# Performance work log

Hardware: AMD Instinct MI355X
Metric: run time of the kernel (lower is better)

The kernel has to match this reference:

```python
import jax, jax.numpy as jnp
import numpy as np

N_QUBITS = 10
N_LAYERS = 3
OUT_MIN, OUT_MAX = -0.1, 0.1


def _apply_1q(state, U, wire):
    # state: (B, 2**n) complex64; U: (2,2) complex64 gate on `wire` (wire 0 = MSB, PennyLane order)
    B = state.shape[0]
    s = state.reshape(B, 2 ** wire, 2, -1)
    s = jnp.einsum('ij,bljr->blir', U, s)
    return s.reshape(B, -1)


def _apply_ry_batched(state, theta, wire):
    # per-sample RY(theta) on `wire`; theta: (B,)
    B = state.shape[0]
    s = state.reshape(B, 2 ** wire, 2, -1)
    c = jnp.cos(0.5 * theta)[:, None, None]
    si = jnp.sin(0.5 * theta)[:, None, None]
    a0, a1 = s[:, :, 0, :], s[:, :, 1, :]
    s = jnp.stack([c * a0 - si * a1, si * a0 + c * a1], axis=2)
    return s.reshape(B, -1)


def _apply_cnot(state, ctrl):
    # CNOT with control=ctrl, target=ctrl+1 (adjacent wires)
    B = state.shape[0]
    s = state.reshape(B, 2 ** ctrl, 2, 2, -1)
    s = jnp.stack([s[:, :, 0], s[:, :, 1, ::-1]], axis=2)
    return s.reshape(B, -1)


def _circuit(z, weights):
    # Faithful statevector simulation of the PennyLane qnode, batched over samples.
    B = z.shape[0]
    n = N_QUBITS
    state = jnp.zeros((B, 2 ** n), jnp.complex64).at[:, 0].set(1.0)
    zc = jnp.clip(z, -1.0, 1.0)
    for i in range(n):
        state = _apply_ry_batched(state, zc[:, i % zc.shape[1]], i)
    # Fuse RZ(a)->RY(b)->RZ(c) per (layer, qubit) into one 2x2 unitary: U = Rz(c) @ Ry(b) @ Rz(a)
    a, b, c = weights[..., 0], weights[..., 1], weights[..., 2]
    ea, eap = jnp.exp(-0.5j * a), jnp.exp(0.5j * a)
    ec, ecp = jnp.exp(-0.5j * c), jnp.exp(0.5j * c)
    cb, sb = jnp.cos(0.5 * b), jnp.sin(0.5 * b)
    U = jnp.stack([jnp.stack([ec * cb * ea, -ec * sb * eap], -1),
                   jnp.stack([ecp * sb * ea, ecp * cb * eap], -1)], -2)  # (L, Q, 2, 2)
    U = U.astype(jnp.complex64)
    for l in range(N_LAYERS):
        for i in range(n):
            state = _apply_1q(state, U[l, i], i)
        for i in range(n - 1):
            state = _apply_cnot(state, i)
    probs = jnp.abs(state) ** 2  # (B, 2**n) float32
    feats = []
    for i in range(n):
        p = probs.reshape(B, 2 ** i, 2, -1)
        feats.append(p[:, :, 0].sum((1, 2)) - p[:, :, 1].sum((1, 2)))  # <Z_i>
    return jnp.stack(feats, -1)  # (B, n_qubits)


def setup_inputs() -> dict:
    key = jax.random.key(0)
    ks = jax.random.split(key, 8)
    B = 4096
    return {
        'z': jax.random.normal(ks[0], (B, N_QUBITS), jnp.float32),
        'weights': jax.random.normal(ks[1], (N_LAYERS, N_QUBITS, 3), jnp.float32) * 0.01,
        'W1': jax.random.normal(ks[2], (N_QUBITS, 32), jnp.float32) * 0.3,
        'b1': jax.random.normal(ks[3], (32,), jnp.float32) * 0.05,
        'W2': jax.random.normal(ks[4], (32, 16), jnp.float32) * 0.2,
        'b2': jax.random.normal(ks[5], (16,), jnp.float32) * 0.05,
        'W3': jax.random.normal(ks[6], (16, 1), jnp.float32) * 0.2,
        'b3': jax.random.normal(ks[7], (1,), jnp.float32) * 0.05,
    }


def reference(z, weights, W1, b1, W2, b2, W3, b3):
    feats = _circuit(z, weights)                  # (B, n_qubits)
    h = jnp.tanh(feats @ W1 + b1)
    h = jnp.tanh(h @ W2 + b2)
    raw = h @ W3 + b3                             # (B, 1)
    return jax.nn.sigmoid(raw) * (OUT_MAX - OUT_MIN) + OUT_MIN
```

## Files before the change

### kernel.cpp

```cpp
#include <hip/hip_runtime.h>

namespace {

constexpr int NQ = 10;

struct cplx { float re, im; };

__device__ __forceinline__ cplx cmul(cplx a, cplx b) {
  cplx r;
  r.re = fmaf(a.re, b.re, -a.im * b.im);
  r.im = fmaf(a.re, b.im,  a.im * b.re);
  return r;
}

__device__ __forceinline__ cplx cmadd2(cplx u, cplx a, cplx v, cplx b) {
  cplx r;
  r.re = fmaf(u.re, a.re, fmaf(-u.im, a.im, fmaf(v.re, b.re, -v.im * b.im)));
  r.im = fmaf(u.re, a.im, fmaf( u.im, a.re, fmaf(v.re, b.im,  v.im * b.re)));
  return r;
}

__device__ __forceinline__ cplx csel(bool c, cplx x, cplx y) {
  cplx r; r.re = c ? x.re : y.re; r.im = c ? x.im : y.im; return r;
}

__device__ __forceinline__ float fast_tanh(float x) {
  float xc = fminf(fmaxf(x, -10.f), 10.f);
  float e = __expf(2.f * xc);
  return __fdividef(e - 1.f, e + 1.f);
}

template<int CTRL>
__device__ __forceinline__ float dppf(float v) {
  return __int_as_float(__builtin_amdgcn_update_dpp(0, __float_as_int(v), CTRL, 0xF, 0xF, true));
}
template<int CTRL>
__device__ __forceinline__ cplx dppc(cplx v) { return { dppf<CTRL>(v.re), dppf<CTRL>(v.im) }; }

__device__ __forceinline__ cplx shflxc(cplx v, int m) {
  cplx r; r.re = __shfl_xor(v.re, m); r.im = __shfl_xor(v.im, m); return r;
}

__device__ __forceinline__ float rdlane(float v, int l) {
  return __int_as_float(__builtin_amdgcn_readlane(__float_as_int(v), l));
}

__device__ __forceinline__ float wave_sum(float v) {
  v += dppf<0xB1>(v);
  v += dppf<0x4E>(v);
  v += __shfl_xor(v, 4);
  v += dppf<0x128>(v);
  v += __shfl_xor(v, 16);
  return rdlane(v, 0) + rdlane(v, 32);
}

__device__ __forceinline__ void loadU(const float* __restrict__ Ut, int g,
                                      cplx& u00, cplx& u01, cplx& u10, cplx& u11) {
  const float* p = Ut + g * 8;
  u00 = {p[0], p[1]}; u01 = {p[2], p[3]};
  u10 = {p[4], p[5]}; u11 = {p[6], p[7]};
}

template<int LX, int HIL>
__device__ __forceinline__ void laneGateDS(cplx (&amp)[16], int lane,
    cplx u00, cplx u01, cplx u10, cplx u11) {
  bool hi = (__popc(lane & HIL) & 1) != 0;
  cplx cA = csel(hi, u11, u00), cB = csel(hi, u10, u01);
  #pragma unroll
  for (int t = 0; t < 16; ++t) {
    cplx o = shflxc(amp[t], LX);
    amp[t] = cmadd2(cA, amp[t], cB, o);
  }
}

template<int CTRL, int HIL>
__device__ __forceinline__ void laneGateDPP(cplx (&amp)[16], int lane,
    cplx u00, cplx u01, cplx u10, cplx u11) {
  bool hi = (__popc(lane & HIL) & 1) != 0;
  cplx cA = csel(hi, u11, u00), cB = csel(hi, u10, u01);
  #pragma unroll
  for (int t = 0; t < 16; ++t) {
    cplx o = dppc<CTRL>(amp[t]);
    amp[t] = cmadd2(cA, amp[t], cB, o);
  }
}

template<int CTRL, int LOCX, int HIL>
__device__ __forceinline__ void mixedGate(cplx (&amp)[16], int lane,
    cplx u00, cplx u01, cplx u10, cplx u11) {
  bool hi = (__popc(lane & HIL) & 1) != 0;
  cplx cA = csel(hi, u11, u00), cB = csel(hi, u10, u01);
  #pragma unroll
  for (int t0 = 0; t0 < 16; ++t0) {
    if (t0 & LOCX) continue;
    const int t1 = t0 | LOCX;
    cplx o0 = dppc<CTRL>(amp[t1]);
    cplx o1 = dppc<CTRL>(amp[t0]);
    amp[t0] = cmadd2(cA, amp[t0], cB, o0);
    amp[t1] = cmadd2(cA, amp[t1], cB, o1);
  }
}

constexpr int hbit(int m) { return m >= 8 ? 8 : (m >= 4 ? 4 : (m >= 2 ? 2 : 1)); }

template<int PLOC, int HIL, int HILOC>
__device__ __forceinline__ void localGate(cplx (&amp)[16], int lane,
    cplx u00, cplx u01, cplx u10, cplx u11) {
  bool h0 = (__popc(lane & HIL) & 1) != 0;
  cplx cA0 = csel(h0, u11, u00), cB0 = csel(h0, u10, u01);
  cplx cA1 = csel(h0, u00, u11), cB1 = csel(h0, u01, u10);
  #pragma unroll
  for (int ta = 0; ta < 16; ++ta) {
    if (ta & hbit(PLOC)) continue;
    const int tb = ta ^ PLOC;
    const bool pa = (__popc(ta & HILOC) & 1) != 0;
    cplx aA = amp[ta], aB = amp[tb];
    if (!pa) {
      amp[ta] = cmadd2(cA0, aA, cB0, aB);
      amp[tb] = cmadd2(cA1, aB, cB1, aA);
    } else {
      amp[ta] = cmadd2(cA1, aA, cB1, aB);
      amp[tb] = cmadd2(cA0, aB, cB0, aA);
    }
  }
}

__global__ void qgan_prep(const float* __restrict__ wts, float* __restrict__ U) {
  int g = threadIdx.x;
  if (g >= 30) return;
  float a = wts[g * 3 + 0], b = wts[g * 3 + 1], c = wts[g * 3 + 2];
  float al = 0.5f * (a + c), be = 0.5f * (a - c), hb = 0.5f * b;
  float ca = cosf(al), sa = sinf(al);
  float cbe = cosf(be), sbe = sinf(be);
  float cb = cosf(hb), sb = sinf(hb);
  float* p = U + g * 8;
  p[0] =  cb * ca;  p[1] = -cb * sa;
  p[2] = -sb * cbe; p[3] = -sb * sbe;
  p[4] =  sb * cbe; p[5] = -sb * sbe;
  p[6] =  cb * ca;  p[7] =  cb * sa;
}

__global__ __launch_bounds__(256, 4)
void qgan_kernel(const float* __restrict__ z, const float* __restrict__ Ut,
                 const float* __restrict__ W1, const float* __restrict__ b1,
                 const float* __restrict__ W2, const float* __restrict__ b2,
                 const float* __restrict__ W3, const float* __restrict__ b3,
                 float* __restrict__ out, int B)
{
  const int tid  = blockIdx.x * 256 + threadIdx.x;
  const int lane = threadIdx.x & 63;
  const int wv   = __builtin_amdgcn_readfirstlane(tid >> 6);
  if (wv >= B) return;

  cplx u00, u01, u10, u11;

  cplx laneF = {1.f, 0.f};
  #pragma unroll
  for (int q = 0; q < 6; ++q) {
    float zz = z[wv * NQ + q];
    zz = fminf(fmaxf(zz, -1.f), 1.f);
    float c0 = __cosf(0.5f * zz), s0 = __sinf(0.5f * zz);
    loadU(Ut, q, u00, u01, u10, u11);
    cplx va = { fmaf(u00.re, c0, u01.re * s0), fmaf(u00.im, c0, u01.im * s0) };
    cplx vb = { fmaf(u10.re, c0, u11.re * s0), fmaf(u10.im, c0, u11.im * s0) };
    cplx f = ((lane >> (5 - q)) & 1) ? vb : va;
    laneF = (q == 0) ? f : cmul(laneF, f);
  }
  cplx va_[4], vb_[4];
  #pragma unroll
  for (int q = 6; q < 10; ++q) {
    float zz = z[wv * NQ + q];
    zz = fminf(fmaxf(zz, -1.f), 1.f);
    float c0 = __cosf(0.5f * zz), s0 = __sinf(0.5f * zz);
    loadU(Ut, q, u00, u01, u10, u11);
    va_[q - 6] = { fmaf(u00.re, c0, u01.re * s0), fmaf(u00.im, c0, u01.im * s0) };
    vb_[q - 6] = { fmaf(u10.re, c0, u11.re * s0), fmaf(u10.im, c0, u11.im * s0) };
  }

  cplx amp[16];
  {
    cplx P2[4];
    P2[0] = cmul(va_[2], va_[3]);
    P2[1] = cmul(va_[2], vb_[3]);
    P2[2] = cmul(vb_[2], va_[3]);
    P2[3] = cmul(vb_[2], vb_[3]);
    cplx g0 = cmul(laneF, va_[0]);
    cplx g1 = cmul(laneF, vb_[0]);
    #pragma unroll
    for (int t = 0; t < 16; ++t) {
      cplx t7 = ((t >> 2) & 1) ? vb_[1] : va_[1];
      cplx tt = cmul(t7, P2[t & 3]);
      amp[t] = cmul(((t >> 3) & 1) ? g1 : g0, tt);
    }
  }

  loadU(Ut, 10, u00,u01,u10,u11); laneGateDS <0x30, 0x20>(amp, lane, u00,u01,u10,u11);
  loadU(Ut, 11, u00,u01,u10,u11); laneGateDS <0x18, 0x30>(amp, lane, u00,u01,u10,u11);
  loadU(Ut, 12, u00,u01,u10,u11); laneGateDS <0x0C, 0x38>(amp, lane, u00,u01,u10,u11);
  loadU(Ut, 13, u00,u01,u10,u11); laneGateDS <0x06, 0x3C>(amp, lane, u00,u01,u10,u11);
  loadU(Ut, 14, u00,u01,u10,u11); laneGateDPP<0x1B, 0x3E>(amp, lane, u00,u01,u10,u11);
  loadU(Ut, 15, u00,u01,u10,u11); mixedGate  <0xB1, 8, 0x3F>(amp, lane, u00,u01,u10,u11);
  loadU(Ut, 16, u00,u01,u10,u11); localGate  <0xC, 0x3F, 0x8>(amp, lane, u00,u01,u10,u11);
  loadU(Ut, 17, u00,u01,u10,u11); localGate  <0x6, 0x3F, 0xC>(amp, lane, u00,u01,u10,u11);
  loadU(Ut, 18, u00,u01,u10,u11); localGate  <0x3, 0x3F, 0xE>(amp, lane, u00,u01,u10,u11);
  loadU(Ut, 19, u00,u01,u10,u11); localGate  <0x1, 0x3F, 0xF>(amp, lane, u00,u01,u10,u11);

  loadU(Ut, 20, u00,u01,u10,u11); laneGateDS <0x28, 0x20>(amp, lane, u00,u01,u10,u11);
  loadU(Ut, 21, u00,u01,u10,u11); laneGateDS <0x14, 0x10>(amp, lane, u00,u01,u10,u11);
  loadU(Ut, 22, u00,u01,u10,u11); laneGateDS <0x0A, 0x28>(amp, lane, u00,u01,u10,u11);
  loadU(Ut, 23, u00,u01,u10,u11); laneGateDS <0x05, 0x14>(amp, lane, u00,u01,u10,u11);
  loadU(Ut, 24, u00,u01,u10,u11); mixedGate  <0x4E, 8, 0x2A>(amp, lane, u00,u01,u10,u11);
  loadU(Ut, 25, u00,u01,u10,u11); mixedGate  <0xB1, 4, 0x15>(amp, lane, u00,u01,u10,u11);
  loadU(Ut, 26, u00,u01,u10,u11); localGate  <0xA, 0x2A, 0x8>(amp, lane, u00,u01,u10,u11);
  loadU(Ut, 27, u00,u01,u10,u11); localGate  <0x5, 0x15, 0x4>(amp, lane, u00,u01,u10,u11);
  loadU(Ut, 28, u00,u01,u10,u11); localGate  <0x2, 0x2A, 0xA>(amp, lane, u00,u01,u10,u11);
  loadU(Ut, 29, u00,u01,u10,u11); localGate  <0x1, 0x15, 0x5>(amp, lane, u00,u01,u10,u11);

  float p[16];
  #pragma unroll
  for (int t = 0; t < 16; ++t)
    p[t] = fmaf(amp[t].re, amp[t].re, amp[t].im * amp[t].im);

  float s0 = 0.f, s8 = 0.f, sC = 0.f, s6 = 0.f, s3 = 0.f;
  #pragma unroll
  for (int t = 0; t < 16; ++t) {
    s0 += p[t];
    s8 += (__popc(t & 0x8) & 1) ? -p[t] : p[t];
    sC += (__popc(t & 0xC) & 1) ? -p[t] : p[t];
    s6 += (__popc(t & 0x6) & 1) ? -p[t] : p[t];
    s3 += (__popc(t & 0x3) & 1) ? -p[t] : p[t];
  }

  const int   lmask[10] = {0x20,0x30,0x18,0x0C,0x26,0x33,0x19,0x0C,0x26,0x33};
  const float lsrc[10]  = {s0,  s0,  s0,  s0,  s0,  s0,  s8,  sC,  s6,  s3 };
  float feats[10];
  #pragma unroll
  for (int w = 0; w < 10; ++w) {
    int par = __popc(lane & lmask[w]) & 1;
    float v = __int_as_float(__float_as_int(lsrc[w]) ^ (par << 31));
    feats[w] = wave_sum(v);
  }

  const int j = lane & 31;
  float acc = b1[j];
  #pragma unroll
  for (int i = 0; i < NQ; ++i) acc = fmaf(feats[i], W1[i * 32 + j], acc);
  float h1 = fast_tanh(acc);

  const int k = lane & 15;
  float acc2 = b2[k];
  #pragma unroll
  for (int jj = 0; jj < 32; ++jj)
    acc2 = fmaf(rdlane(h1, jj), W2[jj * 16 + k], acc2);
  float h2 = fast_tanh(acc2);

  float vv = h2 * W3[k];
  vv += dppf<0xB1>(vv);
  vv += dppf<0x4E>(vv);
  vv += __shfl_xor(vv, 4);
  vv += dppf<0x128>(vv);

  if (lane == 0) out[wv] = 0.1f * fast_tanh(0.5f * (vv + b3[0]));
}

}

extern "C" void kernel_launch(void* const* d_in, const int* in_sizes, int n_in,
                              void* d_out, int out_size, void* d_ws, size_t ws_size,
                              hipStream_t stream) {
  const float* z   = (const float*)d_in[0];
  const float* wts = (const float*)d_in[1];
  const float* W1  = (const float*)d_in[2];
  const float* b1  = (const float*)d_in[3];
  const float* W2  = (const float*)d_in[4];
  const float* b2  = (const float*)d_in[5];
  const float* W3  = (const float*)d_in[6];
  const float* b3  = (const float*)d_in[7];
  float* out = (float*)d_out;
  float* U   = (float*)d_ws;

  int B = in_sizes[0] / NQ;
  hipLaunchKernelGGL(qgan_prep, dim3(1), dim3(32), 0, stream, wts, U);
  int blocks = (B + 3) / 4;
  hipLaunchKernelGGL(qgan_kernel, dim3(blocks), dim3(256), 0, stream,
                     z, U, W1, b1, W2, b2, W3, b3, out, B);
}
```

Before: 93.29 us.

## Use packed float2 math, DPP/swizzle lane exchanges, and fold gate prep into kernel

Complex arithmetic is rewritten on two-wide float vectors so the compiler can emit packed FMA instructions. Several cross-lane shuffles (ds_bpermute-based) are replaced with ds_swizzle or chained DPP moves. The separate prep kernel that built the gate unitaries is removed: each wave computes them per lane and broadcasts them with readlane, which saves a launch and the global loads at the cost of redundant trig per wave. The reductions also swap one shuffle for DPP.

```diff
diff --git a/kernel.cpp b/kernel.cpp
--- a/kernel.cpp
+++ b/kernel.cpp
@@ -4,24 +4,125 @@
 
 constexpr int NQ = 10;
 
-struct cplx { float re, im; };
-
-__device__ __forceinline__ cplx cmul(cplx a, cplx b) {
-  cplx r;
-  r.re = fmaf(a.re, b.re, -a.im * b.im);
-  r.im = fmaf(a.re, b.im,  a.im * b.re);
+typedef float v2f __attribute__((ext_vector_type(2)));
+
+__device__ __forceinline__ float rdlane(float v, int l) {
+  return __int_as_float(__builtin_amdgcn_readlane(__float_as_int(v), l));
+}
+template<int CTRL>
+__device__ __forceinline__ float dppf(float v) {
+  return __int_as_float(__builtin_amdgcn_update_dpp(0, __float_as_int(v), CTRL, 0xF, 0xF, true));
+}
+template<int CTRL>
+__device__ __forceinline__ v2f dppv(v2f v) { return v2f{dppf<CTRL>(v.x), dppf<CTRL>(v.y)}; }
+template<int C1, int C2>
+__device__ __forceinline__ v2f dppv2(v2f v) { return dppv<C2>(dppv<C1>(v)); }
+
+template<int PAT>
+__device__ __forceinline__ v2f swzv(v2f v) {
+  return v2f{ __int_as_float(__builtin_amdgcn_ds_swizzle(__float_as_int(v.x), PAT)),
+              __int_as_float(__builtin_amdgcn_ds_swizzle(__float_as_int(v.y), PAT)) };
+}
+__device__ __forceinline__ v2f shflx(v2f v, int m) {
+  return v2f{ __shfl_xor(v.x, m), __shfl_xor(v.y, m) };
+}
+
+__device__ __forceinline__ v2f pfma(v2f a, v2f b, v2f c) { return __builtin_elementwise_fma(a, b, c); }
+__device__ __forceinline__ v2f swp(v2f a) { return v2f{a.y, a.x}; }
+__device__ __forceinline__ v2f cmulv(v2f a, v2f b) {
+  return pfma(swp(b), v2f{-a.y, a.y}, b * v2f{a.x, a.x});
+}
+__device__ __forceinline__ v2f vsel(bool c, v2f a, v2f b) {
+  return v2f{ c ? a.x : b.x, c ? a.y : b.y };
+}
+struct pkco { v2f rA, iA, rB, iB; };
+__device__ __forceinline__ pkco mkco(v2f cA, v2f cB) {
+  return pkco{ v2f{cA.x, cA.x}, v2f{-cA.y, cA.y}, v2f{cB.x, cB.x}, v2f{-cB.y, cB.y} };
+}
+__device__ __forceinline__ v2f capply(const pkco& c, v2f a, v2f o) {
+  v2f r = a * c.rA;
+  r = pfma(swp(a), c.iA, r);
+  r = pfma(o, c.rB, r);
+  r = pfma(swp(o), c.iB, r);
   return r;
 }
 
-__device__ __forceinline__ cplx cmadd2(cplx u, cplx a, cplx v, cplx b) {
-  cplx r;
-  r.re = fmaf(u.re, a.re, fmaf(-u.im, a.im, fmaf(v.re, b.re, -v.im * b.im)));
-  r.im = fmaf(u.re, a.im, fmaf( u.im, a.re, fmaf(v.re, b.im,  v.im * b.re)));
-  return r;
-}
-
-__device__ __forceinline__ cplx csel(bool c, cplx x, cplx y) {
-  cplx r; r.re = c ? x.re : y.re; r.im = c ? x.im : y.im; return r;
+__device__ __forceinline__ float wave_sum(float v) {
+  v += dppf<0xB1>(v);
+  v += dppf<0x4E>(v);
+  v += dppf<0x1B>(dppf<0x141>(v));
+  v += dppf<0x128>(v);
+  v += __shfl_xor(v, 16);
+  return rdlane(v, 0) + rdlane(v, 32);
+}
+
+struct Umat { float r00,i00,r01,i01,r10,i10,r11,i11; };
+__device__ __forceinline__ void getU(const Umat& m, int g,
+                                     v2f& u00, v2f& u01, v2f& u10, v2f& u11) {
+  u00 = v2f{rdlane(m.r00, g), rdlane(m.i00, g)};
+  u01 = v2f{rdlane(m.r01, g), rdlane(m.i01, g)};
+  u10 = v2f{rdlane(m.r10, g), rdlane(m.i10, g)};
+  u11 = v2f{rdlane(m.r11, g), rdlane(m.i11, g)};
+}
+
+template<int HIL>
+__device__ __forceinline__ pkco gateco(int lane, v2f u00, v2f u01, v2f u10, v2f u11) {
+  bool hi = (__popc(lane & HIL) & 1) != 0;
+  return mkco(vsel(hi, u11, u00), vsel(hi, u10, u01));
+}
+
+template<int LX, int HIL>
+__device__ __forceinline__ void gate_shfl(v2f (&amp)[16], int lane, v2f u00,v2f u01,v2f u10,v2f u11) {
+  pkco c = gateco<HIL>(lane, u00,u01,u10,u11);
+  #pragma unroll
+  for (int t = 0; t < 16; ++t) amp[t] = capply(c, amp[t], shflx(amp[t], LX));
+}
+template<int PAT, int HIL>
+__device__ __forceinline__ void gate_swz(v2f (&amp)[16], int lane, v2f u00,v2f u01,v2f u10,v2f u11) {
+  pkco c = gateco<HIL>(lane, u00,u01,u10,u11);
+  #pragma unroll
+  for (int t = 0; t < 16; ++t) amp[t] = capply(c, amp[t], swzv<PAT>(amp[t]));
+}
+template<int C1, int HIL>
+__device__ __forceinline__ void gate_dpp1(v2f (&amp)[16], int lane, v2f u00,v2f u01,v2f u10,v2f u11) {
+  pkco c = gateco<HIL>(lane, u00,u01,u10,u11);
+  #pragma unroll
+  for (int t = 0; t < 16; ++t) amp[t] = capply(c, amp[t], dppv<C1>(amp[t]));
+}
+template<int C1, int C2, int HIL>
+__device__ __forceinline__ void gate_dpp2(v2f (&amp)[16], int lane, v2f u00,v2f u01,v2f u10,v2f u11) {
+  pkco c = gateco<HIL>(lane, u00,u01,u10,u11);
+  #pragma unroll
+  for (int t = 0; t < 16; ++t) amp[t] = capply(c, amp[t], dppv2<C1,C2>(amp[t]));
+}
+template<int CTRL, int LOCX, int HIL>
+__device__ __forceinline__ void gate_mixed(v2f (&amp)[16], int lane, v2f u00,v2f u01,v2f u10,v2f u11) {
+  pkco c = gateco<HIL>(lane, u00,u01,u10,u11);
+  #pragma unroll
+  for (int t0 = 0; t0 < 16; ++t0) {
+    if (t0 & LOCX) continue;
+    const int t1 = t0 | LOCX;
+    v2f o0 = dppv<CTRL>(amp[t1]);
+    v2f o1 = dppv<CTRL>(amp[t0]);
+    amp[t0] = capply(c, amp[t0], o0);
+    amp[t1] = capply(c, amp[t1], o1);
+  }
+}
+constexpr int hbit(int m) { return m >= 8 ? 8 : (m >= 4 ? 4 : (m >= 2 ? 2 : 1)); }
+template<int PLOC, int HIL, int HILOC>
+__device__ __forceinline__ void gate_local(v2f (&amp)[16], int lane, v2f u00,v2f u01,v2f u10,v2f u11) {
+  bool h0 = (__popc(lane & HIL) & 1) != 0;
+  pkco c0 = mkco(vsel(h0, u11, u00), vsel(h0, u10, u01));
+  pkco c1 = mkco(vsel(h0, u00, u11), vsel(h0, u01, u10));
+  #pragma unroll
+  for (int ta = 0; ta < 16; ++ta) {
+    if (ta & hbit(PLOC)) continue;
+    const int tb = ta ^ PLOC;
+    const bool pa = (__popc(ta & HILOC) & 1) != 0;
+    v2f aA = amp[ta], aB = amp[tb];
+    if (!pa) { amp[ta] = capply(c0, aA, aB); amp[tb] = capply(c1, aB, aA); }
+    else     { amp[ta] = capply(c1, aA, aB); amp[tb] = capply(c0, aB, aA); }
+  }
 }
 
 __device__ __forceinline__ float fast_tanh(float x) {
@@ -30,118 +131,8 @@
   return __fdividef(e - 1.f, e + 1.f);
 }
 
-template<int CTRL>
-__device__ __forceinline__ float dppf(float v) {
-  return __int_as_float(__builtin_amdgcn_update_dpp(0, __float_as_int(v), CTRL, 0xF, 0xF, true));
-}
-template<int CTRL>
-__device__ __forceinline__ cplx dppc(cplx v) { return { dppf<CTRL>(v.re), dppf<CTRL>(v.im) }; }
-
-__device__ __forceinline__ cplx shflxc(cplx v, int m) {
-  cplx r; r.re = __shfl_xor(v.re, m); r.im = __shfl_xor(v.im, m); return r;
-}
-
-__device__ __forceinline__ float rdlane(float v, int l) {
-  return __int_as_float(__builtin_amdgcn_readlane(__float_as_int(v), l));
-}
-
-__device__ __forceinline__ float wave_sum(float v) {
-  v += dppf<0xB1>(v);
-  v += dppf<0x4E>(v);
-  v += __shfl_xor(v, 4);
-  v += dppf<0x128>(v);
-  v += __shfl_xor(v, 16);
-  return rdlane(v, 0) + rdlane(v, 32);
-}
-
-__device__ __forceinline__ void loadU(const float* __restrict__ Ut, int g,
-                                      cplx& u00, cplx& u01, cplx& u10, cplx& u11) {
-  const float* p = Ut + g * 8;
-  u00 = {p[0], p[1]}; u01 = {p[2], p[3]};
-  u10 = {p[4], p[5]}; u11 = {p[6], p[7]};
-}
-
-template<int LX, int HIL>
-__device__ __forceinline__ void laneGateDS(cplx (&amp)[16], int lane,
-    cplx u00, cplx u01, cplx u10, cplx u11) {
-  bool hi = (__popc(lane & HIL) & 1) != 0;
-  cplx cA = csel(hi, u11, u00), cB = csel(hi, u10, u01);
-  #pragma unroll
-  for (int t = 0; t < 16; ++t) {
-    cplx o = shflxc(amp[t], LX);
-    amp[t] = cmadd2(cA, amp[t], cB, o);
-  }
-}
-
-template<int CTRL, int HIL>
-__device__ __forceinline__ void laneGateDPP(cplx (&amp)[16], int lane,
-    cplx u00, cplx u01, cplx u10, cplx u11) {
-  bool hi = (__popc(lane & HIL) & 1) != 0;
-  cplx cA = csel(hi, u11, u00), cB = csel(hi, u10, u01);
-  #pragma unroll
-  for (int t = 0; t < 16; ++t) {
-    cplx o = dppc<CTRL>(amp[t]);
-    amp[t] = cmadd2(cA, amp[t], cB, o);
-  }
-}
-
-template<int CTRL, int LOCX, int HIL>
-__device__ __forceinline__ void mixedGate(cplx (&amp)[16], int lane,
-    cplx u00, cplx u01, cplx u10, cplx u11) {
-  bool hi = (__popc(lane & HIL) & 1) != 0;
-  cplx cA = csel(hi, u11, u00), cB = csel(hi, u10, u01);
-  #pragma unroll
-  for (int t0 = 0; t0 < 16; ++t0) {
-    if (t0 & LOCX) continue;
-    const int t1 = t0 | LOCX;
-    cplx o0 = dppc<CTRL>(amp[t1]);
-    cplx o1 = dppc<CTRL>(amp[t0]);
-    amp[t0] = cmadd2(cA, amp[t0], cB, o0);
-    amp[t1] = cmadd2(cA, amp[t1], cB, o1);
-  }
-}
-
-constexpr int hbit(int m) { return m >= 8 ? 8 : (m >= 4 ? 4 : (m >= 2 ? 2 : 1)); }
-
-template<int PLOC, int HIL, int HILOC>
-__device__ __forceinline__ void localGate(cplx (&amp)[16], int lane,
-    cplx u00, cplx u01, cplx u10, cplx u11) {
-  bool h0 = (__popc(lane & HIL) & 1) != 0;
-  cplx cA0 = csel(h0, u11, u00), cB0 = csel(h0, u10, u01);
-  cplx cA1 = csel(h0, u00, u11), cB1 = csel(h0, u01, u10);
-  #pragma unroll
-  for (int ta = 0; ta < 16; ++ta) {
-    if (ta & hbit(PLOC)) continue;
-    const int tb = ta ^ PLOC;
-    const bool pa = (__popc(ta & HILOC) & 1) != 0;
-    cplx aA = amp[ta], aB = amp[tb];
-    if (!pa) {
-      amp[ta] = cmadd2(cA0, aA, cB0, aB);
-      amp[tb] = cmadd2(cA1, aB, cB1, aA);
-    } else {
-      amp[ta] = cmadd2(cA1, aA, cB1, aB);
-      amp[tb] = cmadd2(cA0, aB, cB0, aA);
-    }
-  }
-}
-
-__global__ void qgan_prep(const float* __restrict__ wts, float* __restrict__ U) {
-  int g = threadIdx.x;
-  if (g >= 30) return;
-  float a = wts[g * 3 + 0], b = wts[g * 3 + 1], c = wts[g * 3 + 2];
-  float al = 0.5f * (a + c), be = 0.5f * (a - c), hb = 0.5f * b;
-  float ca = cosf(al), sa = sinf(al);
-  float cbe = cosf(be), sbe = sinf(be);
-  float cb = cosf(hb), sb = sinf(hb);
-  float* p = U + g * 8;
-  p[0] =  cb * ca;  p[1] = -cb * sa;
-  p[2] = -sb * cbe; p[3] = -sb * sbe;
-  p[4] =  sb * cbe; p[5] = -sb * sbe;
-  p[6] =  cb * ca;  p[7] =  cb * sa;
-}
-
 __global__ __launch_bounds__(256, 4)
-void qgan_kernel(const float* __restrict__ z, const float* __restrict__ Ut,
+void qgan_kernel(const float* __restrict__ z, const float* __restrict__ wts,
                  const float* __restrict__ W1, const float* __restrict__ b1,
                  const float* __restrict__ W2, const float* __restrict__ b2,
                  const float* __restrict__ W3, const float* __restrict__ b3,
@@ -152,75 +143,89 @@
   const int wv   = __builtin_amdgcn_readfirstlane(tid >> 6);
   if (wv >= B) return;
 
-  cplx u00, u01, u10, u11;
-
-  cplx laneF = {1.f, 0.f};
+  Umat m;
+  {
+    int g = (lane < 30) ? lane : 0;
+    float wa = wts[g * 3 + 0], wb = wts[g * 3 + 1], wc = wts[g * 3 + 2];
+    float al = 0.5f * (wa + wc), be = 0.5f * (wa - wc), hb = 0.5f * wb;
+    float ca = __cosf(al),  sa = __sinf(al);
+    float cbe = __cosf(be), sbe = __sinf(be);
+    float cb = __cosf(hb),  sb = __sinf(hb);
+    m.r00 =  cb * ca;  m.i00 = -cb * sa;
+    m.r01 = -sb * cbe; m.i01 = -sb * sbe;
+    m.r10 =  sb * cbe; m.i10 = -sb * sbe;
+    m.r11 =  cb * ca;  m.i11 =  cb * sa;
+  }
+
+  v2f u00, u01, u10, u11;
+  const float* zp = z + wv * NQ;
+
+  v2f laneF = {1.f, 0.f};
   #pragma unroll
   for (int q = 0; q < 6; ++q) {
-    float zz = z[wv * NQ + q];
-    zz = fminf(fmaxf(zz, -1.f), 1.f);
+    float zz = fminf(fmaxf(zp[q], -1.f), 1.f);
     float c0 = __cosf(0.5f * zz), s0 = __sinf(0.5f * zz);
-    loadU(Ut, q, u00, u01, u10, u11);
-    cplx va = { fmaf(u00.re, c0, u01.re * s0), fmaf(u00.im, c0, u01.im * s0) };
-    cplx vb = { fmaf(u10.re, c0, u11.re * s0), fmaf(u10.im, c0, u11.im * s0) };
-    cplx f = ((lane >> (5 - q)) & 1) ? vb : va;
-    laneF = (q == 0) ? f : cmul(laneF, f);
-  }
-  cplx va_[4], vb_[4];
+    getU(m, q, u00, u01, u10, u11);
+    v2f va = pfma(u01, v2f{s0, s0}, u00 * v2f{c0, c0});
+    v2f vb = pfma(u11, v2f{s0, s0}, u10 * v2f{c0, c0});
+    v2f f = vsel((lane >> (5 - q)) & 1, vb, va);
+    laneF = (q == 0) ? f : cmulv(laneF, f);
+  }
+  v2f va_[4], vb_[4];
   #pragma unroll
   for (int q = 6; q < 10; ++q) {
-    float zz = z[wv * NQ + q];
-    zz = fminf(fmaxf(zz, -1.f), 1.f);
+    float zz = fminf(fmaxf(zp[q], -1.f), 1.f);
     float c0 = __cosf(0.5f * zz), s0 = __sinf(0.5f * zz);
-    loadU(Ut, q, u00, u01, u10, u11);
-    va_[q - 6] = { fmaf(u00.re, c0, u01.re * s0), fmaf(u00.im, c0, u01.im * s0) };
-    vb_[q - 6] = { fmaf(u10.re, c0, u11.re * s0), fmaf(u10.im, c0, u11.im * s0) };
-  }
-
-  cplx amp[16];
+    getU(m, q, u00, u01, u10, u11);
+    va_[q - 6] = pfma(u01, v2f{s0, s0}, u00 * v2f{c0, c0});
+    vb_[q - 6] = pfma(u11, v2f{s0, s0}, u10 * v2f{c0, c0});
+  }
+
+  v2f amp[16];
   {
-    cplx P2[4];
-    P2[0] = cmul(va_[2], va_[3]);
-    P2[1] = cmul(va_[2], vb_[3]);
-    P2[2] = cmul(vb_[2], va_[3]);
-    P2[3] = cmul(vb_[2], vb_[3]);
-    cplx g0 = cmul(laneF, va_[0]);
-    cplx g1 = cmul(laneF, vb_[0]);
+    v2f P2[4];
+    P2[0] = cmulv(va_[2], va_[3]);
+    P2[1] = cmulv(va_[2], vb_[3]);
+    P2[2] = cmulv(vb_[2], va_[3]);
+    P2[3] = cmulv(vb_[2], vb_[3]);
+    v2f g0 = cmulv(laneF, va_[0]);
+    v2f g1 = cmulv(laneF, vb_[0]);
     #pragma unroll
     for (int t = 0; t < 16; ++t) {
-      cplx t7 = ((t >> 2) & 1) ? vb_[1] : va_[1];
-      cplx tt = cmul(t7, P2[t & 3]);
-      amp[t] = cmul(((t >> 3) & 1) ? g1 : g0, tt);
+      v2f t7 = ((t >> 2) & 1) ? vb_[1] : va_[1];
+      v2f tt = cmulv(t7, P2[t & 3]);
+      amp[t] = cmulv(((t >> 3) & 1) ? g1 : g0, tt);
     }
   }
 
-  loadU(Ut, 10, u00,u01,u10,u11); laneGateDS <0x30, 0x20>(amp, lane, u00,u01,u10,u11);
-  loadU(Ut, 11, u00,u01,u10,u11); laneGateDS <0x18, 0x30>(amp, lane, u00,u01,u10,u11);
-  loadU(Ut, 12, u00,u01,u10,u11); laneGateDS <0x0C, 0x38>(amp, lane, u00,u01,u10,u11);
-  loadU(Ut, 13, u00,u01,u10,u11); laneGateDS <0x06, 0x3C>(amp, lane, u00,u01,u10,u11);
-  loadU(Ut, 14, u00,u01,u10,u11); laneGateDPP<0x1B, 0x3E>(amp, lane, u00,u01,u10,u11);
-  loadU(Ut, 15, u00,u01,u10,u11); mixedGate  <0xB1, 8, 0x3F>(amp, lane, u00,u01,u10,u11);
-  loadU(Ut, 16, u00,u01,u10,u11); localGate  <0xC, 0x3F, 0x8>(amp, lane, u00,u01,u10,u11);
-  loadU(Ut, 17, u00,u01,u10,u11); localGate  <0x6, 0x3F, 0xC>(amp, lane, u00,u01,u10,u11);
-  loadU(Ut, 18, u00,u01,u10,u11); localGate  <0x3, 0x3F, 0xE>(amp, lane, u00,u01,u10,u11);
-  loadU(Ut, 19, u00,u01,u10,u11); localGate  <0x1, 0x3F, 0xF>(amp, lane, u00,u01,u10,u11);
-
-  loadU(Ut, 20, u00,u01,u10,u11); laneGateDS <0x28, 0x20>(amp, lane, u00,u01,u10,u11);
-  loadU(Ut, 21, u00,u01,u10,u11); laneGateDS <0x14, 0x10>(amp, lane, u00,u01,u10,u11);
-  loadU(Ut, 22, u00,u01,u10,u11); laneGateDS <0x0A, 0x28>(amp, lane, u00,u01,u10,u11);
-  loadU(Ut, 23, u00,u01,u10,u11); laneGateDS <0x05, 0x14>(amp, lane, u00,u01,u10,u11);
-  loadU(Ut, 24, u00,u01,u10,u11); mixedGate  <0x4E, 8, 0x2A>(amp, lane, u00,u01,u10,u11);
-  loadU(Ut, 25, u00,u01,u10,u11); mixedGate  <0xB1, 4, 0x15>(amp, lane, u00,u01,u10,u11);
-  loadU(Ut, 26, u00,u01,u10,u11); localGate  <0xA, 0x2A, 0x8>(amp, lane, u00,u01,u10,u11);
-  loadU(Ut, 27, u00,u01,u10,u11); localGate  <0x5, 0x15, 0x4>(amp, lane, u00,u01,u10,u11);
-  loadU(Ut, 28, u00,u01,u10,u11); localGate  <0x2, 0x2A, 0xA>(amp, lane, u00,u01,u10,u11);
-  loadU(Ut, 29, u00,u01,u10,u11); localGate  <0x1, 0x15, 0x5>(amp, lane, u00,u01,u10,u11);
+  getU(m, 10, u00,u01,u10,u11); gate_shfl <0x30, 0x20>(amp, lane, u00,u01,u10,u11);
+  getU(m, 11, u00,u01,u10,u11); gate_swz  <0x601F, 0x30>(amp, lane, u00,u01,u10,u11);
+  getU(m, 12, u00,u01,u10,u11); gate_dpp2 <0x140, 0x1B, 0x38>(amp, lane, u00,u01,u10,u11);
+  getU(m, 13, u00,u01,u10,u11); gate_dpp2 <0x141, 0xB1, 0x3C>(amp, lane, u00,u01,u10,u11);
+  getU(m, 14, u00,u01,u10,u11); gate_dpp1 <0x1B, 0x3E>(amp, lane, u00,u01,u10,u11);
+  getU(m, 15, u00,u01,u10,u11); gate_mixed<0xB1, 8, 0x3F>(amp, lane, u00,u01,u10,u11);
+  getU(m, 16, u00,u01,u10,u11); gate_local<0xC, 0x3F, 0x8>(amp, lane, u00,u01,u10,u11);
+  getU(m, 17, u00,u01,u10,u11); gate_local<0x6, 0x3F, 0xC>(amp, lane, u00,u01,u10,u11);
+  getU(m, 18, u00,u01,u10,u11); gate_local<0x3, 0x3F, 0xE>(amp, lane, u00,u01,u10,u11);
+  getU(m, 19, u00,u01,u10,u11); gate_local<0x1, 0x3F, 0xF>(amp, lane, u00,u01,u10,u11);
+
+  getU(m, 20, u00,u01,u10,u11); gate_shfl <0x28, 0x20>(amp, lane, u00,u01,u10,u11);
+  getU(m, 21, u00,u01,u10,u11); gate_swz  <0x501F, 0x10>(amp, lane, u00,u01,u10,u11);
+  getU(m, 22, u00,u01,u10,u11); gate_dpp2 <0x128, 0x4E, 0x28>(amp, lane, u00,u01,u10,u11);
+  getU(m, 23, u00,u01,u10,u11); gate_dpp2 <0x141, 0x4E, 0x14>(amp, lane, u00,u01,u10,u11);
+  getU(m, 24, u00,u01,u10,u11); gate_mixed<0x4E, 8, 0x2A>(amp, lane, u00,u01,u10,u11);
+  getU(m, 25, u00,u01,u10,u11); gate_mixed<0xB1, 4, 0x15>(amp, lane, u00,u01,u10,u11);
+  getU(m, 26, u00,u01,u10,u11); gate_local<0xA, 0x2A, 0x8>(amp, lane, u00,u01,u10,u11);
+  getU(m, 27, u00,u01,u10,u11); gate_local<0x5, 0x15, 0x4>(amp, lane, u00,u01,u10,u11);
+  getU(m, 28, u00,u01,u10,u11); gate_local<0x2, 0x2A, 0xA>(amp, lane, u00,u01,u10,u11);
+  getU(m, 29, u00,u01,u10,u11); gate_local<0x1, 0x15, 0x5>(amp, lane, u00,u01,u10,u11);
 
   float p[16];
   #pragma unroll
-  for (int t = 0; t < 16; ++t)
-    p[t] = fmaf(amp[t].re, amp[t].re, amp[t].im * amp[t].im);
-
+  for (int t = 0; t < 16; ++t) {
+    v2f q2 = amp[t] * amp[t];
+    p[t] = q2.x + q2.y;
+  }
   float s0 = 0.f, s8 = 0.f, sC = 0.f, s6 = 0.f, s3 = 0.f;
   #pragma unroll
   for (int t = 0; t < 16; ++t) {
@@ -230,7 +235,6 @@
     s6 += (__popc(t & 0x6) & 1) ? -p[t] : p[t];
     s3 += (__popc(t & 0x3) & 1) ? -p[t] : p[t];
   }
-
   const int   lmask[10] = {0x20,0x30,0x18,0x0C,0x26,0x33,0x19,0x0C,0x26,0x33};
   const float lsrc[10]  = {s0,  s0,  s0,  s0,  s0,  s0,  s8,  sC,  s6,  s3 };
   float feats[10];
@@ -257,7 +261,7 @@
   float vv = h2 * W3[k];
   vv += dppf<0xB1>(vv);
   vv += dppf<0x4E>(vv);
-  vv += __shfl_xor(vv, 4);
+  vv += dppf<0x1B>(dppf<0x141>(vv));
   vv += dppf<0x128>(vv);
 
   if (lane == 0) out[wv] = 0.1f * fast_tanh(0.5f * (vv + b3[0]));
@@ -277,11 +281,10 @@
   const float* W3  = (const float*)d_in[6];
   const float* b3  = (const float*)d_in[7];
   float* out = (float*)d_out;
-  float* U   = (float*)d_ws;
+  (void)d_ws; (void)ws_size;
 
   int B = in_sizes[0] / NQ;
-  hipLaunchKernelGGL(qgan_prep, dim3(1), dim3(32), 0, stream, wts, U);
   int blocks = (B + 3) / 4;
   hipLaunchKernelGGL(qgan_kernel, dim3(blocks), dim3(256), 0, stream,
-                     z, U, W1, b1, W2, b2, W3, b3, out, B);
-}
+                     z, wts, W1, b1, W2, b2, W3, b3, out, B);
+}
```

Measured after the change: 88.36 us. 5.3% less time.
